# Performance work log

Measured on AMD Instinct MI355X. Metric: run time of the kernel, lower is better.

## Reference

```python
import jax, jax.numpy as jnp
import numpy as np

B, T = 1024, 8192


def setup_inputs() -> dict:
    key = jax.random.key(0)
    k1, k2 = jax.random.split(key)
    # phi/psi are [B, T, 2] probability-bound robustness traces in [0, 1]
    phi = jax.random.uniform(k1, (B, T, 2), dtype=jnp.float32)
    psi = jax.random.uniform(k2, (B, T, 2), dtype=jnp.float32)
    return {"phi": phi, "psi": psi}


def reference(phi, psi):
    """Until operator, interval [0, inf), exact (scale<=0) min/max.

    Original O(T^2) double loop computes, for each t:
        out[t] = max_{tau in [t, T-1]} min( min(phi[t..tau-1]), psi[tau] )
    with the empty segment (tau == t) contributing min(ones, psi[t]).
    Because min distributes over max, this satisfies the exact O(T)
    backward recurrence:
        r[t] = max( min(1, psi[t]), min(phi[t], r[t+1]) ),  r[T] = -inf
    which we evaluate with a reversed lax.scan over the time axis.
    """
    phi_t = jnp.swapaxes(phi, 0, 1)  # [T, B, 2]
    psi_t = jnp.swapaxes(psi, 0, 1)  # [T, B, 2]

    def step(carry, xs):
        p, q = xs
        v = jnp.minimum(jnp.asarray(1.0, p.dtype), q)  # tau == t term (min with ones)
        r = jnp.maximum(v, jnp.minimum(p, carry))
        return r, r

    init = jnp.full(phi_t.shape[1:], -jnp.inf, dtype=phi.dtype)  # [B, 2]
    _, out = jax.lax.scan(step, init, (phi_t, psi_t), reverse=True)
    return jnp.swapaxes(out, 0, 1)  # [B, T, 2]
```

## Files before the change

kernel.cpp:

```cpp
#include <hip/hip_runtime.h>


#define T_LEN 8192
#define NW    16
#define BLOCK (NW * 64)

__device__ __forceinline__ float rfl(float x) {
    return __int_as_float(__builtin_amdgcn_readfirstlane(__float_as_int(x)));
}

__device__ __forceinline__ void wave_lds_fence() {
    __asm__ volatile("" ::: "memory");
    __builtin_amdgcn_wave_barrier();
    __asm__ volatile("" ::: "memory");
}

__global__ __launch_bounds__(BLOCK, 8) void until_kernel(
    const float* __restrict__ phi, const float* __restrict__ psi,
    float* __restrict__ out)
{
    const int  row  = blockIdx.x;
    const int  tid  = threadIdx.x;
    const int  w    = tid >> 6;
    const int  lane = tid & 63;
    const float NEG = -__builtin_huge_valf();
    const float POS =  __builtin_huge_valf();

    const size_t segf4 = (size_t)row * (T_LEN / 2) + (size_t)w * 256;
    const float4* __restrict__ phi4 = (const float4*)phi + segf4;
    const float4* __restrict__ psi4 = (const float4*)psi + segf4;
    float4* __restrict__ out4 = (float4*)out + segf4;

    __shared__ alignas(16) float lds[NW * 1024];
    __shared__ float4 ssum[NW];
    float* wl = lds + w * 1024;

    {
        float4 P[4], Q[4];
#pragma unroll
        for (int k = 0; k < 4; ++k) {
            P[k] = phi4[k * 64 + lane];
            Q[k] = psi4[k * 64 + lane];
        }

#pragma unroll
        for (int k = 0; k < 4; ++k) {
            float* base = wl + k * 64 + lane;
            float v0x = fminf(1.f, Q[k].x), v0y = fminf(1.f, Q[k].y);
            float v1x = fminf(1.f, Q[k].z), v1y = fminf(1.f, Q[k].w);
            base[0]   = fmaxf(v0x, fminf(P[k].x, v1x));
            base[256] = fmaxf(v0y, fminf(P[k].y, v1y));
            base[512] = fminf(P[k].x, P[k].z);
            base[768] = fminf(P[k].y, P[k].w);
        }
    }
    wave_lds_fence();

    float4 GAx, GAy, GBx, GBy;
    GAx = *(const float4*)(wl + 0 * 256 + lane * 4);
    GAy = *(const float4*)(wl + 1 * 256 + lane * 4);
    GBx = *(const float4*)(wl + 2 * 256 + lane * 4);
    GBy = *(const float4*)(wl + 3 * 256 + lane * 4);

    float hax = GAx.w, hay = GAy.w, hbx = GBx.w, hby = GBy.w;
    hax = fmaxf(GAx.z, fminf(GBx.z, hax));
    hay = fmaxf(GAy.z, fminf(GBy.z, hay));
    hbx = fminf(GBx.z, hbx);
    hby = fminf(GBy.z, hby);
    hax = fmaxf(GAx.y, fminf(GBx.y, hax));
    hay = fmaxf(GAy.y, fminf(GBy.y, hay));
    hbx = fminf(GBx.y, hbx);
    hby = fminf(GBy.y, hby);
    hax = fmaxf(GAx.x, fminf(GBx.x, hax));
    hay = fmaxf(GAy.x, fminf(GBy.x, hay));
    hbx = fminf(GBx.x, hbx);
    hby = fminf(GBy.x, hby);

#pragma unroll
    for (int off = 1; off < 64; off <<= 1) {
        float gax = __shfl_down(hax, off), gay = __shfl_down(hay, off);
        float gbx = __shfl_down(hbx, off), gby = __shfl_down(hby, off);
        bool  val = (lane + off) < 64;
        gax = val ? gax : NEG;  gay = val ? gay : NEG;
        gbx = val ? gbx : POS;  gby = val ? gby : POS;
        hax = fmaxf(hax, fminf(hbx, gax));
        hay = fmaxf(hay, fminf(hby, gay));
        hbx = fminf(hbx, gbx);
        hby = fminf(hby, gby);
    }
    const float Sax = hax, Say = hay, Sbx = hbx, Sby = hby;

    if (lane == 0) ssum[w] = make_float4(Sax, Say, Sbx, Sby);
    __syncthreads();
    float rcx = NEG, rcy = NEG;
    for (int j = NW - 1; j > w; --j) {
        float4 s = ssum[j];
        rcx = fmaxf(s.x, fminf(s.z, rcx));
        rcy = fmaxf(s.y, fminf(s.w, rcy));
    }

    {
        float yx = fmaxf(Sax, fminf(Sbx, rcx));
        float yy = fmaxf(Say, fminf(Sby, rcy));
        float cx = __shfl_down(yx, 1), cy = __shfl_down(yy, 1);
        if (lane == 63) { cx = rcx; cy = rcy; }
        float4 CX, CY;
        CX.w = cx;
        CY.w = cy;
        CX.z = fmaxf(GAx.w, fminf(GBx.w, CX.w));
        CY.z = fmaxf(GAy.w, fminf(GBy.w, CY.w));
        CX.y = fmaxf(GAx.z, fminf(GBx.z, CX.z));
        CY.y = fmaxf(GAy.z, fminf(GBy.z, CY.z));
        CX.x = fmaxf(GAx.y, fminf(GBx.y, CX.y));
        CY.x = fmaxf(GAy.y, fminf(GBy.y, CY.y));
        *(float4*)(wl +       lane * 4) = CX;
        *(float4*)(wl + 256 + lane * 4) = CY;
    }
    wave_lds_fence();

#pragma unroll
    for (int k = 0; k < 4; ++k) {
        const int e = k * 64 + lane;
        float4 P2 = phi4[e];
        float4 Q2 = psi4[e];
        float cx = wl[e];
        float cy = wl[256 + e];
        float r1x = fmaxf(fminf(1.f, Q2.z), fminf(P2.z, cx));
        float r1y = fmaxf(fminf(1.f, Q2.w), fminf(P2.w, cy));
        float r0x = fmaxf(fminf(1.f, Q2.x), fminf(P2.x, r1x));
        float r0y = fmaxf(fminf(1.f, Q2.y), fminf(P2.y, r1y));
        out4[e] = make_float4(r0x, r0y, r1x, r1y);
    }
}

extern "C" void kernel_launch(void* const* d_in, const int* in_sizes, int n_in,
                              void* d_out, int out_size, void* d_ws, size_t ws_size,
                              hipStream_t stream) {
    const float* phi = (const float*)d_in[0];
    const float* psi = (const float*)d_in[1];
    float* out = (float*)d_out;
    const int Bn = in_sizes[0] / (T_LEN * 2);
    until_kernel<<<Bn, BLOCK, 0, stream>>>(phi, psi, out);
}
```

Measured before the change: 179.9 us.

## Keep per-lane contiguous chunk in registers, drop LDS transpose and global reload

Each lane now loads 4 consecutive float4s (a contiguous chunk of 8 timesteps) and keeps phi and clamped psi in registers. It computes its chunk summary directly and, after the cross-lane and cross-wave scan, runs the final backward pass from registers. This removes the LDS staging and transpose and the second global read of phi and psi, which halves input traffic. In exchange, each lane's loads use a 64-byte stride instead of fully coalesced 16-byte-per-lane accesses, and register pressure goes up.

```diff
diff --git a/kernel.cpp b/kernel.cpp
--- a/kernel.cpp
+++ b/kernel.cpp
@@ -4,16 +4,6 @@
 #define T_LEN 8192
 #define NW    16
 #define BLOCK (NW * 64)
-
-__device__ __forceinline__ float rfl(float x) {
-    return __int_as_float(__builtin_amdgcn_readfirstlane(__float_as_int(x)));
-}
-
-__device__ __forceinline__ void wave_lds_fence() {
-    __asm__ volatile("" ::: "memory");
-    __builtin_amdgcn_wave_barrier();
-    __asm__ volatile("" ::: "memory");
-}
 
 __global__ __launch_bounds__(BLOCK, 8) void until_kernel(
     const float* __restrict__ phi, const float* __restrict__ psi,
@@ -26,55 +16,43 @@
     const float NEG = -__builtin_huge_valf();
     const float POS =  __builtin_huge_valf();
 
-    const size_t segf4 = (size_t)row * (T_LEN / 2) + (size_t)w * 256;
-    const float4* __restrict__ phi4 = (const float4*)phi + segf4;
-    const float4* __restrict__ psi4 = (const float4*)psi + segf4;
-    float4* __restrict__ out4 = (float4*)out + segf4;
+    const size_t base = (size_t)row * (T_LEN / 2) + (size_t)w * 256
+                      + (size_t)lane * 4;
+    const float4* __restrict__ phi4 = (const float4*)phi + base;
+    const float4* __restrict__ psi4 = (const float4*)psi + base;
+    float4* __restrict__ out4 = (float4*)out + base;
 
-    __shared__ alignas(16) float lds[NW * 1024];
     __shared__ float4 ssum[NW];
-    float* wl = lds + w * 1024;
 
-    {
-        float4 P[4], Q[4];
+    float4 P[4], V[4];
 #pragma unroll
-        for (int k = 0; k < 4; ++k) {
-            P[k] = phi4[k * 64 + lane];
-            Q[k] = psi4[k * 64 + lane];
-        }
+    for (int k = 0; k < 4; ++k) {
+        P[k] = phi4[k];
+        V[k] = psi4[k];
+    }
+#pragma unroll
+    for (int k = 0; k < 4; ++k) {
+        V[k].x = fminf(1.f, V[k].x);
+        V[k].y = fminf(1.f, V[k].y);
+        V[k].z = fminf(1.f, V[k].z);
+        V[k].w = fminf(1.f, V[k].w);
+    }
 
+    float hax = fmaxf(V[3].x, fminf(P[3].x, V[3].z));
+    float hay = fmaxf(V[3].y, fminf(P[3].y, V[3].w));
+    float hbx = fminf(P[3].x, P[3].z);
+    float hby = fminf(P[3].y, P[3].w);
 #pragma unroll
-        for (int k = 0; k < 4; ++k) {
-            float* base = wl + k * 64 + lane;
-            float v0x = fminf(1.f, Q[k].x), v0y = fminf(1.f, Q[k].y);
-            float v1x = fminf(1.f, Q[k].z), v1y = fminf(1.f, Q[k].w);
-            base[0]   = fmaxf(v0x, fminf(P[k].x, v1x));
-            base[256] = fmaxf(v0y, fminf(P[k].y, v1y));
-            base[512] = fminf(P[k].x, P[k].z);
-            base[768] = fminf(P[k].y, P[k].w);
-        }
+    for (int k = 2; k >= 0; --k) {
+        float ax = fmaxf(V[k].x, fminf(P[k].x, V[k].z));
+        float ay = fmaxf(V[k].y, fminf(P[k].y, V[k].w));
+        float bx = fminf(P[k].x, P[k].z);
+        float by = fminf(P[k].y, P[k].w);
+        hax = fmaxf(ax, fminf(bx, hax));
+        hay = fmaxf(ay, fminf(by, hay));
+        hbx = fminf(bx, hbx);
+        hby = fminf(by, hby);
     }
-    wave_lds_fence();
-
-    float4 GAx, GAy, GBx, GBy;
-    GAx = *(const float4*)(wl + 0 * 256 + lane * 4);
-    GAy = *(const float4*)(wl + 1 * 256 + lane * 4);
-    GBx = *(const float4*)(wl + 2 * 256 + lane * 4);
-    GBy = *(const float4*)(wl + 3 * 256 + lane * 4);
-
-    float hax = GAx.w, hay = GAy.w, hbx = GBx.w, hby = GBy.w;
-    hax = fmaxf(GAx.z, fminf(GBx.z, hax));
-    hay = fmaxf(GAy.z, fminf(GBy.z, hay));
-    hbx = fminf(GBx.z, hbx);
-    hby = fminf(GBy.z, hby);
-    hax = fmaxf(GAx.y, fminf(GBx.y, hax));
-    hay = fmaxf(GAy.y, fminf(GBy.y, hay));
-    hbx = fminf(GBx.y, hbx);
-    hby = fminf(GBy.y, hby);
-    hax = fmaxf(GAx.x, fminf(GBx.x, hax));
-    hay = fmaxf(GAy.x, fminf(GBy.x, hay));
-    hbx = fminf(GBx.x, hbx);
-    hby = fminf(GBy.x, hby);
 
 #pragma unroll
     for (int off = 1; off < 64; off <<= 1) {
@@ -99,37 +77,20 @@
         rcy = fmaxf(s.y, fminf(s.w, rcy));
     }
 
-    {
-        float yx = fmaxf(Sax, fminf(Sbx, rcx));
-        float yy = fmaxf(Say, fminf(Sby, rcy));
-        float cx = __shfl_down(yx, 1), cy = __shfl_down(yy, 1);
-        if (lane == 63) { cx = rcx; cy = rcy; }
-        float4 CX, CY;
-        CX.w = cx;
-        CY.w = cy;
-        CX.z = fmaxf(GAx.w, fminf(GBx.w, CX.w));
-        CY.z = fmaxf(GAy.w, fminf(GBy.w, CY.w));
-        CX.y = fmaxf(GAx.z, fminf(GBx.z, CX.z));
-        CY.y = fmaxf(GAy.z, fminf(GBy.z, CY.z));
-        CX.x = fmaxf(GAx.y, fminf(GBx.y, CX.y));
-        CY.x = fmaxf(GAy.y, fminf(GBy.y, CY.y));
-        *(float4*)(wl +       lane * 4) = CX;
-        *(float4*)(wl + 256 + lane * 4) = CY;
-    }
-    wave_lds_fence();
+    float yx = fmaxf(Sax, fminf(Sbx, rcx));
+    float yy = fmaxf(Say, fminf(Sby, rcy));
+    float cx = __shfl_down(yx, 1), cy = __shfl_down(yy, 1);
+    if (lane == 63) { cx = rcx; cy = rcy; }
 
 #pragma unroll
-    for (int k = 0; k < 4; ++k) {
-        const int e = k * 64 + lane;
-        float4 P2 = phi4[e];
-        float4 Q2 = psi4[e];
-        float cx = wl[e];
-        float cy = wl[256 + e];
-        float r1x = fmaxf(fminf(1.f, Q2.z), fminf(P2.z, cx));
-        float r1y = fmaxf(fminf(1.f, Q2.w), fminf(P2.w, cy));
-        float r0x = fmaxf(fminf(1.f, Q2.x), fminf(P2.x, r1x));
-        float r0y = fmaxf(fminf(1.f, Q2.y), fminf(P2.y, r1y));
-        out4[e] = make_float4(r0x, r0y, r1x, r1y);
+    for (int k = 3; k >= 0; --k) {
+        float r1x = fmaxf(V[k].z, fminf(P[k].z, cx));
+        float r1y = fmaxf(V[k].w, fminf(P[k].w, cy));
+        float r0x = fmaxf(V[k].x, fminf(P[k].x, r1x));
+        float r0y = fmaxf(V[k].y, fminf(P[k].y, r1y));
+        out4[k] = make_float4(r0x, r0y, r1x, r1y);
+        cx = r0x;
+        cy = r0y;
     }
 }
 
```

New measurement: 176.4 us. No clear change (-2.0%).
